# Kernel tuning notes

Hardware: AMD Instinct MI355X
Metric: run time of the kernel (lower is better)

The kernel has to match this reference:

```python
import jax, jax.numpy as jnp
import numpy as np

B, C, H, W = 8, 256, 64, 64
CK = 64  # C // k with k=4


def setup_inputs() -> dict:
    key = jax.random.key(0)
    ks = jax.random.split(key, 5)
    s = 1.0 / np.sqrt(C)
    return {
        "x": jax.random.normal(ks[0], (B, C, H, W), dtype=jnp.float32),
        "wq": jax.random.normal(ks[1], (CK, C), dtype=jnp.float32) * s,
        "bq": jnp.zeros((CK,), dtype=jnp.float32),
        "wk": jax.random.normal(ks[2], (CK, C), dtype=jnp.float32) * s,
        "bk": jnp.zeros((CK,), dtype=jnp.float32),
        "wv": jax.random.normal(ks[3], (C, C), dtype=jnp.float32) * s,
        "bv": jnp.zeros((C,), dtype=jnp.float32),
        "wg": jax.random.normal(ks[4], (C, C), dtype=jnp.float32) * s,
        "bg": jnp.zeros((C,), dtype=jnp.float32),
    }


def reference(x, wq, bq, wk, bk, wv, bv, wg, bg):
    b, c, h, w = x.shape
    n = h * w
    xf = x.reshape(b, c, n)  # [B, C, N]
    # 1x1 convs are channel-wise matmuls
    q = jnp.einsum('oc,bcn->bon', wq, xf) + bq[None, :, None]  # [B, Ck, N]
    k = jnp.einsum('oc,bcn->bon', wk, xf) + bk[None, :, None]  # [B, Ck, N]
    v = jnp.einsum('oc,bcn->bon', wv, xf) + bv[None, :, None]  # [B, C, N]
    # energy[b,i,j] = q[b,:,i] . k[b,:,j]
    energy = jnp.einsum('bci,bcj->bij', q, k)  # [B, N, N]
    energy = jax.nn.elu(energy) / n
    out = jnp.einsum('bcn,bnj->bcj', v, energy).reshape(b, c, h, w)
    out = jnp.einsum('oc,bchw->bohw', wg, out) + bg[None, :, None, None]
    return out
```

## Files before the change

### kernel.cpp

```cpp
#include <hip/hip_runtime.h>
#include <math.h>

#define BATCH 8
#define CH    256
#define NPIX  4096
#define CKDIM 64

typedef __attribute__((ext_vector_type(8))) short short8;
typedef __attribute__((ext_vector_type(4))) float f32x4;

#define MFMA16x16(a, b, c) __builtin_amdgcn_mfma_f32_16x16x32_bf16((a), (b), (c), 0, 0, 0)

__device__ __forceinline__ unsigned short f2bf(float f) {
    union { float f; unsigned int u; } v; v.f = f;
    unsigned int u = v.u;
    u += 0x7fffu + ((u >> 16) & 1u);
    return (unsigned short)(u >> 16);
}

__global__ void prep_kernel(const float* __restrict__ wq, const float* __restrict__ bq,
                            const float* __restrict__ wk, const float* __restrict__ bk,
                            const float* __restrict__ wv, const float* __restrict__ bv,
                            const float* __restrict__ wg,
                            unsigned short* __restrict__ W_frag, float* __restrict__ bias_all) {
    int o = blockIdx.x;
    int c = threadIdx.x;

    float val;
    if (o < 64) {
        val = wq[o * CH + c];
        if (c == 0) bias_all[o] = bq[o];
    } else if (o < 128) {
        int oo = o - 64;
        val = wk[oo * CH + c];
        if (c == 0) bias_all[o] = bk[oo];
    } else {
        __shared__ float wgr[CH];
        int oo = o - 128;
        wgr[c] = wg[oo * CH + c];
        __syncthreads();
        float a0 = 0.f, a1 = 0.f, a2 = 0.f, a3 = 0.f;
#pragma unroll 4
        for (int m = 0; m < CH; m += 4) {
            a0 += wgr[m + 0] * wv[(m + 0) * CH + c];
            a1 += wgr[m + 1] * wv[(m + 1) * CH + c];
            a2 += wgr[m + 2] * wv[(m + 2) * CH + c];
            a3 += wgr[m + 3] * wv[(m + 3) * CH + c];
        }
        val = (a0 + a1) + (a2 + a3);
        if (c == 0) {
            float b = 0.f;
            for (int m = 0; m < CH; ++m) b += wgr[m] * bv[m];
            bias_all[o] = b;
        }
    }

    int og = o >> 6, w = (o >> 4) & 3, col = o & 15;
    int kc = c >> 5, quad = (c >> 3) & 3, e = c & 7;
    size_t idx = ((size_t)(((og * 4 + w) * 8 + kc) * 64 + quad * 16 + col)) * 8 + e;
    W_frag[idx] = f2bf(val);
}

__global__ __launch_bounds__(256, 3)
void qkvf_mfma(const float* __restrict__ x,
               const unsigned short* __restrict__ W_frag,
               const float* __restrict__ bias_all,
               unsigned short* __restrict__ qk, unsigned short* __restrict__ vp) {
    __shared__ float Tl[64][65];
    __shared__ __align__(16) unsigned short Xl[64][264];

    int n0   = blockIdx.x * 64;
    int b    = blockIdx.y;
    int tid  = threadIdx.x;
    int lane = tid & 63;
    int w    = tid >> 6;
    int col  = lane & 15;
    int quad = lane >> 4;

    for (int c0 = 0; c0 < CH; c0 += 64) {
        if (c0) __syncthreads();
#pragma unroll
        for (int r = 0; r < 4; ++r) {
            int f  = r * 256 + tid;
            int c  = f >> 4;
            int n4 = f & 15;
            float4 v = *(const float4*)(x + ((size_t)b * CH + c0 + c) * NPIX + n0 + n4 * 4);
            Tl[n4 * 4 + 0][c] = v.x;
            Tl[n4 * 4 + 1][c] = v.y;
            Tl[n4 * 4 + 2][c] = v.z;
            Tl[n4 * 4 + 3][c] = v.w;
        }
        __syncthreads();
#pragma unroll
        for (int r = 0; r < 2; ++r) {
            int f    = r * 256 + tid;
            int nrow = f >> 3;
            int c8   = f & 7;
            unsigned int pk[4];
#pragma unroll
            for (int p = 0; p < 4; ++p) {
                unsigned int lo = f2bf(Tl[nrow][c8 * 8 + p * 2 + 0]);
                unsigned int hi = f2bf(Tl[nrow][c8 * 8 + p * 2 + 1]);
                pk[p] = lo | (hi << 16);
            }
            *(uint4*)&Xl[nrow][c0 + c8 * 8] = *(uint4*)pk;
        }
    }
    __syncthreads();

#pragma unroll
    for (int og = 0; og < 6; ++og) {
        int o0 = og * 64;
        const unsigned short* Af = W_frag + ((size_t)(og * 32 + w * 8) << 9);

        f32x4 acc[4];
#pragma unroll
        for (int t = 0; t < 4; ++t) acc[t] = (f32x4){0.f, 0.f, 0.f, 0.f};

#pragma unroll
        for (int kc = 0; kc < 8; ++kc) {
            short8 a = *(const short8*)(Af + ((kc << 6) + lane) * 8);
#pragma unroll
            for (int nt = 0; nt < 4; ++nt) {
                short8 bb = *(const short8*)&Xl[nt * 16 + col][kc * 32 + quad * 8];
                acc[nt] = MFMA16x16(a, bb, acc[nt]);
            }
        }

        float4 bias = *(const float4*)(bias_all + o0 + w * 16 + quad * 4);
        float bs[4] = {bias.x, bias.y, bias.z, bias.w};

        if (og < 2) {
#pragma unroll
            for (int nt = 0; nt < 4; ++nt) {
                int n = n0 + nt * 16 + col;
                unsigned int pk[2];
#pragma unroll
                for (int p = 0; p < 2; ++p) {
                    unsigned int lo = f2bf(acc[nt][p * 2 + 0] + bs[p * 2 + 0]);
                    unsigned int hi = f2bf(acc[nt][p * 2 + 1] + bs[p * 2 + 1]);
                    pk[p] = lo | (hi << 16);
                }
                *(uint2*)(qk + ((size_t)b * NPIX + n) * 128 + o0 + w * 16 + quad * 4) = *(uint2*)pk;
            }
        } else {
#pragma unroll
            for (int nt = 0; nt < 4; ++nt) {
                int n = n0 + nt * 16 + col;
#pragma unroll
                for (int r = 0; r < 4; ++r) {
                    int oo = o0 - 128 + w * 16 + quad * 4 + r;
                    vp[((size_t)b * CH + oo) * NPIX + n] = f2bf((acc[nt][r] + bs[r]) * (1.0f / 4096.0f));
                }
            }
        }
    }
}

#define LPK 72
__global__ __launch_bounds__(512, 4)
void attn_v15(const unsigned short* __restrict__ qk,
              const unsigned short* __restrict__ vp,
              const float* __restrict__ bg, float* __restrict__ out) {
    __shared__ __align__(16) unsigned short Qt[2][64][LPK];
    __shared__ __align__(16) unsigned short St[2][64][LPK];

    int lin  = blockIdx.y * gridDim.x + blockIdx.x;
    int b    = lin & 7;
    int j0   = (lin >> 3) * 64;
    int tid  = threadIdx.x;
    int lane = tid & 63;
    int w    = tid >> 6;
    int col  = lane & 15;
    int quad = lane >> 4;

    int tjA = w & 3;
    int tiP = (w >> 2) * 2;

    short8 bK[2];
#pragma unroll
    for (int ks = 0; ks < 2; ++ks)
        bK[ks] = *(const short8*)(qk + ((size_t)b * NPIX + j0 + tjA * 16 + col) * 128 + 64 + ks * 32 + quad * 8);

    f32x4 acc[2][4];
#pragma unroll
    for (int ot = 0; ot < 2; ++ot)
#pragma unroll
        for (int tj = 0; tj < 4; ++tj) acc[ot][tj] = (f32x4){0.f, 0.f, 0.f, 0.f};

    int qrow = tid >> 3, q8 = tid & 7;
    const unsigned short* Qsrc = qk + ((size_t)b * NPIX + qrow) * 128 + q8 * 8;
    const unsigned short* Vsrc[2];
#pragma unroll
    for (int ot = 0; ot < 2; ++ot)
        Vsrc[ot] = vp + ((size_t)b * CH + (w * 2 + ot) * 16 + col) * NPIX + quad * 8;

    {
        uint4 q0 = *(const uint4*)Qsrc;
        *(uint4*)&Qt[0][qrow][q8 * 8] = q0;
    }
    uint4 qrA = *(const uint4*)(Qsrc + (size_t)64 * 128);
    short8 vb[2][2];
#pragma unroll
    for (int ot = 0; ot < 2; ++ot)
#pragma unroll
        for (int ks = 0; ks < 2; ++ks)
            vb[ot][ks] = *(const short8*)(Vsrc[ot] + ks * 32);

    __syncthreads();

#pragma unroll
    for (int t = 0; t < 2; ++t) {
        int ti = tiP + t;
        short8 a0 = *(const short8*)&Qt[0][ti * 16 + col][quad * 8];
        short8 a1 = *(const short8*)&Qt[0][ti * 16 + col][32 + quad * 8];
        f32x4 s = (f32x4){0.f, 0.f, 0.f, 0.f};
        s = MFMA16x16(a0, bK[0], s);
        s = MFMA16x16(a1, bK[1], s);
        unsigned int pk2[2];
#pragma unroll
        for (int pp = 0; pp < 2; ++pp) {
            float e0 = s[pp * 2 + 0];
            float e1 = s[pp * 2 + 1];
            float g0 = __expf(e0) - 1.f;
            float g1 = __expf(e1) - 1.f;
            e0 = (e0 > 0.f) ? e0 : g0;
            e1 = (e1 > 0.f) ? e1 : g1;
            unsigned int rpk;
            asm("v_cvt_pk_bf16_f32 %0, %1, %2" : "=v"(rpk) : "v"(e0), "v"(e1));
            pk2[pp] = rpk;
        }
        *(uint2*)&St[0][tjA * 16 + col][ti * 16 + quad * 4] = *(uint2*)pk2;
    }
    *(uint4*)&Qt[1][qrow][q8 * 8] = qrA;
    qrA = *(const uint4*)(Qsrc + (size_t)(2 * 64) * 128);

    for (int it = 1; it < NPIX / 64; ++it) {
        int pw = it & 1;

        __syncthreads();

        *(uint4*)&Qt[pw ^ 1][qrow][q8 * 8] = qrA;

        {
            size_t iq = (size_t)(((it + 2) * 64) & (NPIX - 1));
            qrA = *(const uint4*)(Qsrc + iq * 128);
        }
        int iv = it * 64;
        short8 vb_n[2][2];
#pragma unroll
        for (int ot = 0; ot < 2; ++ot)
#pragma unroll
            for (int ks = 0; ks < 2; ++ks)
                vb_n[ot][ks] = *(const short8*)(Vsrc[ot] + iv + ks * 32);

#pragma unroll
        for (int ks = 0; ks < 2; ++ks) {
            short8 sb[4];
#pragma unroll
            for (int tj = 0; tj < 4; ++tj)
                sb[tj] = *(const short8*)&St[pw ^ 1][tj * 16 + col][ks * 32 + quad * 8];
            __builtin_amdgcn_s_setprio(1);
#pragma unroll
            for (int ot = 0; ot < 2; ++ot)
#pragma unroll
                for (int tj = 0; tj < 4; ++tj)
                    acc[ot][tj] = MFMA16x16(sb[tj], vb[ot][ks], acc[ot][tj]);
            __builtin_amdgcn_s_setprio(0);
        }

#pragma unroll
        for (int t = 0; t < 2; ++t) {
            int ti = tiP + t;
            short8 a0 = *(const short8*)&Qt[pw][ti * 16 + col][quad * 8];
            short8 a1 = *(const short8*)&Qt[pw][ti * 16 + col][32 + quad * 8];
            f32x4 s = (f32x4){0.f, 0.f, 0.f, 0.f};
            s = MFMA16x16(a0, bK[0], s);
            s = MFMA16x16(a1, bK[1], s);
            unsigned int pk2[2];
#pragma unroll
            for (int pp = 0; pp < 2; ++pp) {
                float e0 = s[pp * 2 + 0];
                float e1 = s[pp * 2 + 1];
                float g0 = __expf(e0) - 1.f;
                float g1 = __expf(e1) - 1.f;
                e0 = (e0 > 0.f) ? e0 : g0;
                e1 = (e1 > 0.f) ? e1 : g1;
                unsigned int rpk;
                asm("v_cvt_pk_bf16_f32 %0, %1, %2" : "=v"(rpk) : "v"(e0), "v"(e1));
                pk2[pp] = rpk;
            }
            *(uint2*)&St[pw][tjA * 16 + col][ti * 16 + quad * 4] = *(uint2*)pk2;
        }

#pragma unroll
        for (int ot = 0; ot < 2; ++ot)
#pragma unroll
            for (int ks = 0; ks < 2; ++ks)
                vb[ot][ks] = vb_n[ot][ks];
    }

    __syncthreads();
#pragma unroll
    for (int ks = 0; ks < 2; ++ks) {
        short8 sb[4];
#pragma unroll
        for (int tj = 0; tj < 4; ++tj)
            sb[tj] = *(const short8*)&St[1][tj * 16 + col][ks * 32 + quad * 8];
#pragma unroll
        for (int ot = 0; ot < 2; ++ot)
#pragma unroll
            for (int tj = 0; tj < 4; ++tj)
                acc[ot][tj] = MFMA16x16(sb[tj], vb[ot][ks], acc[ot][tj]);
    }

#pragma unroll
    for (int ot = 0; ot < 2; ++ot) {
        int o = (w * 2 + ot) * 16 + col;
        float bgv = bg[o];
#pragma unroll
        for (int tj = 0; tj < 4; ++tj) {
            int j = j0 + tj * 16 + quad * 4;
            float4 st;
            st.x = acc[ot][tj][0] + bgv;
            st.y = acc[ot][tj][1] + bgv;
            st.z = acc[ot][tj][2] + bgv;
            st.w = acc[ot][tj][3] + bgv;
            *(float4*)&out[((size_t)b * CH + o) * NPIX + j] = st;
        }
    }
}

extern "C" void kernel_launch(void* const* d_in, const int* in_sizes, int n_in,
                              void* d_out, int out_size, void* d_ws, size_t ws_size,
                              hipStream_t stream) {
    const float* x  = (const float*)d_in[0];
    const float* wq = (const float*)d_in[1];
    const float* bq = (const float*)d_in[2];
    const float* wk = (const float*)d_in[3];
    const float* bk = (const float*)d_in[4];
    const float* wv = (const float*)d_in[5];
    const float* bv = (const float*)d_in[6];
    const float* wg = (const float*)d_in[7];
    const float* bg = (const float*)d_in[8];
    float* out = (float*)d_out;

    unsigned short* W_frag = (unsigned short*)d_ws;
    float* bias_all = (float*)(W_frag + 384 * 256);
    unsigned short* qk = (unsigned short*)(bias_all + 384);
    unsigned short* vp = qk + (size_t)BATCH * NPIX * 128;

    prep_kernel<<<dim3(384), dim3(256), 0, stream>>>(wq, bq, wk, bk, wv, bv, wg, W_frag, bias_all);
    qkvf_mfma<<<dim3(NPIX / 64, BATCH), dim3(256), 0, stream>>>(x, W_frag, bias_all, qk, vp);
    attn_v15<<<dim3(NPIX / 64, BATCH), dim3(512), 0, stream>>>(qk, vp, bg, out);
}
```

Before: 245.5 us.

## Split attention reduction over key dimension in two halves with atomic accumulation

Splits the inner loop over the pixel (reduction) dimension into two halves, doubling the grid to 1024 blocks. Each half accumulates partial results into a zeroed output with float atomicAdd, and only the first half adds the bias. The launch bounds are raised to 8 blocks per SM to improve occupancy and balance across CUs. This costs an extra memset of the 32 MB output and atomic traffic, and it recomputes the ELU energy tiles that each half needs.

New measurement: 903.4 us. +268.1%, slower.

```diff
diff --git a/kernel.cpp b/kernel.cpp
--- a/kernel.cpp
+++ b/kernel.cpp
@@ -158,16 +158,18 @@
 }
 
 #define LPK 72
-__global__ __launch_bounds__(512, 4)
-void attn_v15(const unsigned short* __restrict__ qk,
+__global__ __launch_bounds__(512, 8)
+void attn_v16(const unsigned short* __restrict__ qk,
               const unsigned short* __restrict__ vp,
               const float* __restrict__ bg, float* __restrict__ out) {
     __shared__ __align__(16) unsigned short Qt[2][64][LPK];
     __shared__ __align__(16) unsigned short St[2][64][LPK];
 
-    int lin  = blockIdx.y * gridDim.x + blockIdx.x;
-    int b    = lin & 7;
-    int j0   = (lin >> 3) * 64;
+    int lin   = blockIdx.x;
+    int b     = lin & 7;
+    int j0    = ((lin >> 3) & 63) * 64;
+    int ihalf = lin >> 9;
+    int ibase = ihalf * (NPIX / 2);
     int tid  = threadIdx.x;
     int lane = tid & 63;
     int w    = tid >> 6;
@@ -189,11 +191,13 @@
         for (int tj = 0; tj < 4; ++tj) acc[ot][tj] = (f32x4){0.f, 0.f, 0.f, 0.f};
 
     int qrow = tid >> 3, q8 = tid & 7;
-    const unsigned short* Qsrc = qk + ((size_t)b * NPIX + qrow) * 128 + q8 * 8;
+    const unsigned short* Qsrc = qk + ((size_t)b * NPIX + ibase + qrow) * 128 + q8 * 8;
     const unsigned short* Vsrc[2];
 #pragma unroll
     for (int ot = 0; ot < 2; ++ot)
-        Vsrc[ot] = vp + ((size_t)b * CH + (w * 2 + ot) * 16 + col) * NPIX + quad * 8;
+        Vsrc[ot] = vp + ((size_t)b * CH + (w * 2 + ot) * 16 + col) * NPIX + ibase + quad * 8;
+
+    const int NITER = NPIX / 2 / 64;
 
     {
         uint4 q0 = *(const uint4*)Qsrc;
@@ -235,7 +239,7 @@
     *(uint4*)&Qt[1][qrow][q8 * 8] = qrA;
     qrA = *(const uint4*)(Qsrc + (size_t)(2 * 64) * 128);
 
-    for (int it = 1; it < NPIX / 64; ++it) {
+    for (int it = 1; it < NITER; ++it) {
         int pw = it & 1;
 
         __syncthreads();
@@ -243,7 +247,7 @@
         *(uint4*)&Qt[pw ^ 1][qrow][q8 * 8] = qrA;
 
         {
-            size_t iq = (size_t)(((it + 2) * 64) & (NPIX - 1));
+            size_t iq = (size_t)(((it + 2) * 64) & (NPIX / 2 - 1));
             qrA = *(const uint4*)(Qsrc + iq * 128);
         }
         int iv = it * 64;
@@ -317,16 +321,15 @@
 #pragma unroll
     for (int ot = 0; ot < 2; ++ot) {
         int o = (w * 2 + ot) * 16 + col;
-        float bgv = bg[o];
+        float bgv = (ihalf == 0) ? bg[o] : 0.f;
 #pragma unroll
         for (int tj = 0; tj < 4; ++tj) {
             int j = j0 + tj * 16 + quad * 4;
-            float4 st;
-            st.x = acc[ot][tj][0] + bgv;
-            st.y = acc[ot][tj][1] + bgv;
-            st.z = acc[ot][tj][2] + bgv;
-            st.w = acc[ot][tj][3] + bgv;
-            *(float4*)&out[((size_t)b * CH + o) * NPIX + j] = st;
+            float* dst = &out[((size_t)b * CH + o) * NPIX + j];
+            atomicAdd(dst + 0, acc[ot][tj][0] + bgv);
+            atomicAdd(dst + 1, acc[ot][tj][1] + bgv);
+            atomicAdd(dst + 2, acc[ot][tj][2] + bgv);
+            atomicAdd(dst + 3, acc[ot][tj][3] + bgv);
         }
     }
 }
@@ -352,5 +355,6 @@
 
     prep_kernel<<<dim3(384), dim3(256), 0, stream>>>(wq, bq, wk, bk, wv, bv, wg, W_frag, bias_all);
     qkvf_mfma<<<dim3(NPIX / 64, BATCH), dim3(256), 0, stream>>>(x, W_frag, bias_all, qk, vp);
-    attn_v15<<<dim3(NPIX / 64, BATCH), dim3(512), 0, stream>>>(qk, vp, bg, out);
-}
+    hipMemsetAsync(out, 0, (size_t)BATCH * CH * NPIX * sizeof(float), stream);
+    attn_v16<<<dim3(NPIX / 64 * BATCH * 2), dim3(512), 0, stream>>>(qk, vp, bg, out);
+}
```
